# Performance work log

Hardware: AMD Instinct MI355X
Metric: run time of the kernel (lower is better)

## Reference

```python
import jax, jax.numpy as jnp
import numpy as np

B, C, H, W = 4, 64, 64, 64  # x shape; mask is (B,1,8H,8W)


def _conv(x, w, pad=0):
    return jax.lax.conv_general_dilated(
        x, w, (1, 1), [(pad, pad), (pad, pad)],
        dimension_numbers=('NCHW', 'OIHW', 'NCHW'))


def _inorm(x, eps=1e-5):  # InstanceNorm2d, affine=False, biased var (torch default)
    mu = x.mean(axis=(2, 3), keepdims=True)
    var = x.var(axis=(2, 3), keepdims=True)
    return (x - mu) * jax.lax.rsqrt(var + eps)


def _forward(x, mask, kconv_w1, kconv_w2, fs_w1, fs_w2, fs_b2, fs_fuse_w):
    b, c, h, w = x.shape
    n = h * w
    # MaxPool2d(8,8) then binarize
    m = jax.lax.reduce_window(mask, -jnp.inf, jax.lax.max,
                              (1, 1, 8, 8), (1, 1, 8, 8), 'VALID')
    m = (m > 0).astype(x.dtype)
    back = 1.0 - m
    # ResidualBlock K_conv (shared for K and Q paths in original code)
    y = jax.nn.relu(_inorm(_conv(x, kconv_w1, pad=1)))
    y = _inorm(_conv(y, kconv_w2, pad=1))
    kx = jax.nn.relu(y + x)
    # L2-normalized K/Q over channel dim
    K = (kx * back).reshape(b, c, n)
    K = K / (jnp.linalg.norm(K, axis=1, keepdims=True) + 1e-8)
    Q = (kx * m).reshape(b, c, n)
    Q = Q / (jnp.linalg.norm(Q, axis=1, keepdims=True) + 1e-8)
    V = (x * back).reshape(b, c, n)
    # cosine-similarity score map, temperature 20
    score = jnp.einsum('bcq,bck->bqk', Q, K) * 20.0  # (b, n_q, n_k)
    qm = m.reshape(b, 1, n)      # query mask (foreground)
    km = back.reshape(b, 1, n)   # key mask (background)
    NEG = -1000000.0
    validx = score + (1.0 - km) * NEG + (1.0 - qm.transpose(0, 2, 1)) * NEG
    att = jax.nn.softmax(validx, axis=-1) * (qm.transpose(0, 2, 1) * km)
    # att_fore[b,c,q] = sum_k V[b,c,k] * att[b,q,k]
    att_fore = jnp.einsum('bck,bqk->bcq', V, att).reshape(b, c, h, w)
    # Fusion_score
    feat1 = _conv(jnp.concatenate([x * m, att_fore * m], axis=1), fs_w1)
    s = jax.nn.sigmoid(_conv(feat1, fs_w2) + fs_b2[None, :, None, None])
    fused = _conv(jnp.concatenate([x * m, att_fore * m * (1.0 - s)], axis=1), fs_fuse_w)
    fs_out = fused * m + x * (1.0 - m)
    out = fs_out * m + x * (1.0 - m)
    # visualization attention mask
    visatt = att.sum(axis=1).reshape(b, 1, h, w)
    attmask = jnp.repeat(jnp.repeat(visatt, 8, axis=2), 8, axis=3)  # nearest upsample x8
    attmask = attmask / attmask.max()
    return out, attmask


def setup_inputs() -> dict:
    key = jax.random.key(0)
    ks = jax.random.split(key, 8)

    def wgt(k, shape, fan_in):
        return jax.random.normal(k, shape, jnp.float32) / np.sqrt(fan_in)

    x = jax.random.normal(ks[0], (B, C, H, W), jnp.float32)
    # sparse foreground mask so maxpool(8x8)>0 yields a mixed fg/bg mask
    mask = (jax.random.uniform(ks[1], (B, 1, H * 8, W * 8)) < 0.01).astype(jnp.float32)
    return dict(
        x=x, mask=mask,
        kconv_w1=wgt(ks[2], (C, C, 3, 3), C * 9),
        kconv_w2=wgt(ks[3], (C, C, 3, 3), C * 9),
        fs_w1=wgt(ks[4], (C, 2 * C, 1, 1), 2 * C),
        fs_w2=wgt(ks[5], (C, C, 1, 1), C),
        fs_b2=jnp.zeros((C,), jnp.float32),
        fs_fuse_w=wgt(ks[6], (C, 2 * C, 1, 1), 2 * C),
    )


def reference(x, mask, kconv_w1, kconv_w2, fs_w1, fs_w2, fs_b2, fs_fuse_w):
    return _forward(x, mask, kconv_w1, kconv_w2, fs_w1, fs_w2, fs_b2, fs_fuse_w)
```

## Files before the change

kernel.cpp:

```cpp
#include <hip/hip_runtime.h>
#include <hip/hip_bf16.h>

typedef __hip_bfloat16 bf16;
typedef __attribute__((ext_vector_type(8))) short short8;
typedef __attribute__((ext_vector_type(4))) float f32x4;
typedef __attribute__((ext_vector_type(16))) float f32x16;

#define BB 4
#define CC 64
#define NN 4096
#define MH 512
#define MW 512
#define LS 72
#define NPARTS 16
#define NDEN 32

#define WB_AFC  ((size_t)0)
#define WB_VIS  ((size_t)4259840)
#define WB_QIX  ((size_t)4325376)
#define WB_KIX  ((size_t)4390912)
#define WB_MFL  ((size_t)4456448)
#define WB_CNT  ((size_t)4472832)
#define WB_WT1  ((size_t)4476992)
#define WB_WT2  ((size_t)4550720)
#define WB_WFB  ((size_t)4624448)
#define WB_KC   ((size_t)5242880)
#define WB_XT   ((size_t)8388608)
#define WB_KXT  ((size_t)10485760)
#define WB_VC   ((size_t)12582912)
#define WB_QC   ((size_t)14680064)
#define WB_E    ((size_t)16777216)
#define EB_ELEM ((size_t)16777216)
#define WB_AFCP ((size_t)150994944)
#define WB_DENP ((size_t)218103808)
#define WB_VISP ((size_t)220200960)
#define WB_GST  ((size_t)220725248)

__device__ __forceinline__ float us2f(unsigned short u) { return __uint_as_float(((unsigned)u) << 16); }
__device__ __forceinline__ unsigned short f2bu(float f) {
  bf16 h = __float2bfloat16(f);
  return *(unsigned short*)&h;
}

__global__ __launch_bounds__(256) void k_pre(const float* __restrict__ x,
                                             const float* __restrict__ mask,
                                             const float* __restrict__ w1,
                                             const float* __restrict__ w2,
                                             const float* __restrict__ fw1,
                                             const float* __restrict__ fw2,
                                             const float* __restrict__ fwf,
                                             float* __restrict__ outp,
                                             unsigned short* __restrict__ xt,
                                             unsigned char* __restrict__ mfl,
                                             float* __restrict__ vis,
                                             unsigned int* __restrict__ vmaxb,
                                             unsigned short* __restrict__ wT1,
                                             unsigned short* __restrict__ wT2,
                                             unsigned short* __restrict__ wfb) {
  __shared__ float lx[64][65];
  int t = threadIdx.x;
  if (blockIdx.x < 256) {
    int b = blockIdx.x >> 6, p0 = (blockIdx.x & 63) * 64;
    const float* xb = x + (size_t)b * CC * NN + p0;
    float* ob = outp + (size_t)b * CC * NN + p0;
    for (int idx = t; idx < 4096; idx += 256) {
      int c = idx >> 6, j = idx & 63;
      float v = xb[c * NN + j];
      lx[j][c] = v;
      ob[c * NN + j] = v;
    }
    __syncthreads();
    unsigned short* xo = xt + ((size_t)b * NN + p0) * 64;
    for (int idx = t; idx < 2048; idx += 256) {
      int j = idx >> 5, c2 = (idx & 31) * 2;
      ushort2 w2v;
      w2v.x = f2bu(lx[j][c2]);
      w2v.y = f2bu(lx[j][c2 + 1]);
      *(ushort2*)&xo[j * 64 + c2] = w2v;
    }
  } else {
    int g = (blockIdx.x - 256) * 256 + t;
    int o = g >> 2, sub = g & 3;
    int b = o >> 12, p = o & 4095;
    int py = p >> 6, px = p & 63;
    const float* mb = mask + (size_t)b * MH * MW + (py * 8 + sub * 2) * MW + px * 8;
    float mx = 0.f;
    #pragma unroll
    for (int dy = 0; dy < 2; ++dy) {
      const float4* r4 = (const float4*)(mb + dy * MW);
      float4 a = r4[0], c = r4[1];
      mx = fmaxf(mx, fmaxf(fmaxf(a.x, a.y), fmaxf(a.z, a.w)));
      mx = fmaxf(mx, fmaxf(fmaxf(c.x, c.y), fmaxf(c.z, c.w)));
    }
    mx = fmaxf(mx, __shfl_xor(mx, 1));
    mx = fmaxf(mx, __shfl_xor(mx, 2));
    if (sub == 0) {
      mfl[o] = (mx > 0.f) ? 1 : 0;
      vis[o] = 0.f;
    }
    if (g == 0) vmaxb[0] = 0u;
    if (g < 36864) {
      int tap = g >> 12;
      int rem = g & 4095;
      int co = rem >> 6, ci = rem & 63;
      int src = (co * 64 + ci) * 9 + tap;
      wT1[g] = f2bu(w1[src]);
      wT2[g] = f2bu(w2[src]);
    } else if (g < 57344) {
      int j2 = g - 36864;
      if (j2 < 8192)       wfb[j2] = f2bu(fw1[j2]);
      else if (j2 < 12288) wfb[j2] = f2bu(fw2[j2 - 8192]);
      else                 wfb[j2] = f2bu(fwf[j2 - 12288]);
    }
  }
}

__global__ __launch_bounds__(256) void k_compact(const unsigned char* __restrict__ mfl,
                                                 int* __restrict__ qidx, int* __restrict__ kidx,
                                                 int* __restrict__ nq, int* __restrict__ nk) {
  int b = blockIdx.x;
  __shared__ unsigned char lm[4096];
  int t = threadIdx.x;
  *(uint4*)&lm[t * 16] = *(const uint4*)&mfl[b * NN + t * 16];
  __syncthreads();
  if (t >= 64) return;
  int lane = t;
  int qb = 0, kb = 0;
  #pragma unroll
  for (int it = 0; it < 64; ++it) {
    int p = it * 64 + lane;
    bool f = lm[p] != 0;
    unsigned long long bal = __ballot(f);
    int before = __popcll(bal & ((1ULL << lane) - 1ULL));
    if (f)  qidx[b * NN + qb + before] = p;
    if (!f) kidx[b * NN + kb + (lane - before)] = p;
    int cnt = __popcll(bal);
    qb += cnt; kb += 64 - cnt;
  }
  if (lane == 0) { nq[b] = qb; nk[b] = kb; }
}

template <bool NORM_IN>
__global__ __launch_bounds__(256) void k_convm(const unsigned short* __restrict__ src,
                                               const unsigned short* __restrict__ wT,
                                               const float* __restrict__ insum,
                                               const float* __restrict__ insq,
                                               unsigned short* __restrict__ dst,
                                               float* __restrict__ gsump,
                                               float* __restrict__ gsqp) {
  int b = blockIdx.y;
  int r = blockIdx.x;
  __shared__ unsigned short bx[198 * LS];
  __shared__ float nmean[64], ninv[64];
  int t = threadIdx.x;
  if (NORM_IN) {
    if (t < 64) {
      float s = 0.f, s2v = 0.f;
      #pragma unroll 8
      for (int r2 = 0; r2 < 64; ++r2) {
        s   += insum[((size_t)r2 * BB + b) * 64 + t];
        s2v += insq [((size_t)r2 * BB + b) * 64 + t];
      }
      float m = s * (1.f / NN);
      float v = fmaxf(s2v * (1.f / NN) - m * m, 0.f);
      nmean[t] = m; ninv[t] = rsqrtf(v + 1e-5f);
    }
    __syncthreads();
  }
  const unsigned short* sb = src + (size_t)b * NN * 64;
  for (int idx = t; idx < 198 * 8; idx += 256) {
    int row = idx >> 3, c8 = (idx & 7) * 8;
    int dy = row / 66;
    int cx = row - dy * 66 - 1;
    int rr = r + dy - 1;
    uint4 v = make_uint4(0u, 0u, 0u, 0u);
    if ((unsigned)rr < 64u && (unsigned)cx < 64u) {
      v = *(const uint4*)(sb + ((size_t)(rr * 64 + cx)) * 64 + c8);
      if (NORM_IN) {
        unsigned short* e = (unsigned short*)&v;
        #pragma unroll
        for (int j = 0; j < 8; ++j)
          e[j] = f2bu(fmaxf((us2f(e[j]) - nmean[c8 + j]) * ninv[c8 + j], 0.f));
      }
    }
    *(uint4*)&bx[row * LS + c8] = v;
  }
  __syncthreads();
  int lane = t & 63;
  int quad = lane >> 4, col = lane & 15;
  int qw = (t >> 6) * 16;
  f32x4 acc[4] = {{0.f,0.f,0.f,0.f},{0.f,0.f,0.f,0.f},{0.f,0.f,0.f,0.f},{0.f,0.f,0.f,0.f}};
  #pragma unroll
  for (int tap = 0; tap < 9; ++tap) {
    int dy = tap / 3, dx = tap - dy * 3 - 1;
    const unsigned short* wrow = wT + ((size_t)tap * 64 + qw + col) * 64;
    short8 a0 = *(const short8*)(wrow + quad * 8);
    short8 a1 = *(const short8*)(wrow + 32 + quad * 8);
    int rbase = dy * 66 + dx + 1;
    #pragma unroll
    for (int nt = 0; nt < 4; ++nt) {
      int row = rbase + nt * 16 + col;
      short8 b0 = *(const short8*)&bx[row * LS + quad * 8];
      short8 b1 = *(const short8*)&bx[row * LS + 32 + quad * 8];
      acc[nt] = __builtin_amdgcn_mfma_f32_16x16x32_bf16(a0, b0, acc[nt], 0, 0, 0);
      acc[nt] = __builtin_amdgcn_mfma_f32_16x16x32_bf16(a1, b1, acc[nt], 0, 0, 0);
    }
  }
  #pragma unroll
  for (int rr = 0; rr < 4; ++rr) {
    float s1 = acc[0][rr] + acc[1][rr] + acc[2][rr] + acc[3][rr];
    float s2 = acc[0][rr]*acc[0][rr] + acc[1][rr]*acc[1][rr]
             + acc[2][rr]*acc[2][rr] + acc[3][rr]*acc[3][rr];
    s1 += __shfl_xor(s1, 1); s2 += __shfl_xor(s2, 1);
    s1 += __shfl_xor(s1, 2); s2 += __shfl_xor(s2, 2);
    s1 += __shfl_xor(s1, 4); s2 += __shfl_xor(s2, 4);
    s1 += __shfl_xor(s1, 8); s2 += __shfl_xor(s2, 8);
    if (col == 0) {
      int co = qw + quad * 4 + rr;
      gsump[((size_t)r * BB + b) * 64 + co] = s1;
      gsqp [((size_t)r * BB + b) * 64 + co] = s2;
    }
  }
  __syncthreads();
  #pragma unroll
  for (int nt = 0; nt < 4; ++nt)
    #pragma unroll
    for (int rr = 0; rr < 4; ++rr)
      bx[(nt * 16 + col) * LS + qw + quad * 4 + rr] = f2bu(acc[nt][rr]);
  __syncthreads();
  unsigned short* db = dst + ((size_t)b * NN + r * 64) * 64;
  for (int idx = t; idx < 512; idx += 256) {
    int px = idx >> 3, c8 = (idx & 7) * 8;
    *(uint4*)(db + (size_t)px * 64 + c8) = *(const uint4*)&bx[px * LS + c8];
  }
}

__global__ __launch_bounds__(256) void k_knorm(unsigned short* __restrict__ kxt,
                                               const unsigned short* __restrict__ xt,
                                               const float* __restrict__ gsump,
                                               const float* __restrict__ gsqp) {
  int b = blockIdx.x >> 6;
  int p0 = (blockIdx.x & 63) * 64;
  __shared__ float m2[64], i2[64];
  int t = threadIdx.x;
  if (t < 64) {
    float s = 0.f, s2v = 0.f;
    #pragma unroll 8
    for (int r2 = 0; r2 < 64; ++r2) {
      s   += gsump[((size_t)r2 * BB + b) * 64 + t];
      s2v += gsqp [((size_t)r2 * BB + b) * 64 + t];
    }
    float m = s * (1.f / NN);
    float v = fmaxf(s2v * (1.f / NN) - m * m, 0.f);
    m2[t] = m; i2[t] = rsqrtf(v + 1e-5f);
  }
  __syncthreads();
  int px = t >> 2, c0 = (t & 3) * 16;
  size_t base = ((size_t)b * NN + p0 + px) * 64 + c0;
  unsigned short kv[16], xv[16];
  *(uint4*)&kv[0] = *(const uint4*)(kxt + base);
  *(uint4*)&kv[8] = *(const uint4*)(kxt + base + 8);
  *(uint4*)&xv[0] = *(const uint4*)(xt + base);
  *(uint4*)&xv[8] = *(const uint4*)(xt + base + 8);
  float v[16]; float ss = 0.f;
  #pragma unroll
  for (int j = 0; j < 16; ++j) {
    float f = fmaxf((us2f(kv[j]) - m2[c0 + j]) * i2[c0 + j] + us2f(xv[j]), 0.f);
    v[j] = f; ss += f * f;
  }
  ss += __shfl_xor(ss, 1);
  ss += __shfl_xor(ss, 2);
  float inv = 1.f / (sqrtf(ss) + 1e-8f);
  #pragma unroll
  for (int j = 0; j < 16; ++j) kv[j] = f2bu(v[j] * inv);
  *(uint4*)(kxt + base) = *(const uint4*)&kv[0];
  *(uint4*)(kxt + base + 8) = *(const uint4*)&kv[8];
}

__global__ __launch_bounds__(256) void k_gath(const unsigned short* __restrict__ khat,
                                              const unsigned short* __restrict__ xt,
                                              const int* __restrict__ qidx, const int* __restrict__ kidx,
                                              const int* __restrict__ nqv, const int* __restrict__ nkv,
                                              unsigned short* __restrict__ kc,
                                              unsigned short* __restrict__ vc,
                                              unsigned short* __restrict__ qc) {
  int b = blockIdx.y;
  int j0 = blockIdx.x * 64;
  int nqb = nqv[b], nkb = nkv[b];
  int NKP = (nkb + 63) & ~63, NQP = (nqb + 63) & ~63;
  bool dok = j0 < NKP, doq = j0 < NQP;
  if (!dok && !doq) return;
  __shared__ int li[128];
  int t = threadIdx.x;
  if (t < 64)       li[t]      = (j0 + t < nkb) ? kidx[b * NN + j0 + t] : -1;
  else if (t < 128) li[t - 64 + 64] = li[t - 64 + 64];
  if (t >= 64 && t < 128) li[t] = (j0 + (t - 64) < nqb) ? qidx[b * NN + j0 + (t - 64)] : -1;
  __syncthreads();
  const unsigned short* khb = khat + (size_t)b * NN * 64;
  const unsigned short* xtb = xt + (size_t)b * NN * 64;
  uint4 z = make_uint4(0u, 0u, 0u, 0u);
  for (int idx = t; idx < 512; idx += 256) {
    int row = idx >> 3, c8 = (idx & 7) * 8;
    size_t dsto = ((size_t)b * NN + j0 + row) * 64 + c8;
    if (dok) {
      int sk = li[row];
      *(uint4*)(kc + dsto) = (sk >= 0) ? *(const uint4*)(khb + (size_t)sk * 64 + c8) : z;
      *(uint4*)(vc + dsto) = (sk >= 0) ? *(const uint4*)(xtb + (size_t)sk * 64 + c8) : z;
    }
    if (doq) {
      int sq = li[64 + row];
      *(uint4*)(qc + dsto) = (sq >= 0) ? *(const uint4*)(khb + (size_t)sq * 64 + c8) : z;
    }
  }
}

__global__ __launch_bounds__(256) void k_att1(const unsigned short* __restrict__ kc,
                                              const unsigned short* __restrict__ vc,
                                              const unsigned short* __restrict__ qc,
                                              const int* __restrict__ nqv, const int* __restrict__ nkv,
                                              float* __restrict__ afc_part, float* __restrict__ den_part,
                                              unsigned short* __restrict__ eg) {
  int b = blockIdx.y;
  int nqb = nqv[b], nkb = nkv[b];
  int q0 = (blockIdx.x >> 4) * 64;
  int part = blockIdx.x & (NPARTS - 1);
  if (q0 >= nqb) return;
  int ntiles = (nkb + 63) >> 6;
  int nt_blk = (part < ntiles) ? ((ntiles - part + NPARTS - 1) >> 4) : 0;
  int NKP = (nkb + 63) & ~63;
  __shared__ unsigned short lk [64 * LS];
  __shared__ unsigned short lvT[64 * LS];
  __shared__ unsigned short le [64 * LS];
  int t = threadIdx.x;
  int wave = t >> 6, lane = t & 63;
  int l31 = lane & 31, lhi = lane >> 5;
  int qh = wave >> 1, kh = wave & 1;
  const unsigned short* kcb = kc + (size_t)b * NN * 64;
  const unsigned short* vcb = vc + (size_t)b * NN * 64;
  const unsigned short* qcb = qc + (size_t)b * NN * 64;
  unsigned short* egb = eg + (size_t)b * EB_ELEM;
  float* afcp = afc_part + (((size_t)part * BB + b) * NN) * 64;
  float* denp = den_part + (((size_t)(part * 2 + kh)) * BB + b) * NN;
  int qq_a = q0 + qh * 32 + l31;
  short8 aq[4];
  #pragma unroll
  for (int ks = 0; ks < 4; ++ks)
    aq[ks] = *(const short8*)(qcb + (size_t)qq_a * 64 + ks * 16 + lhi * 8);
  int klo = t >> 3, c8 = (t & 7) * 8, vcc = t & 7;
  uint4 g0, g1, g2, g3;
  auto issue_gather = [&](int it) {
    int j0 = (part + it * NPARTS) * 64;
    g0 = *(const uint4*)(kcb + (size_t)(j0 + klo) * 64 + c8);
    g1 = *(const uint4*)(kcb + (size_t)(j0 + klo + 32) * 64 + c8);
    g2 = *(const uint4*)(vcb + (size_t)(j0 + 2 * klo) * 64 + c8);
    g3 = *(const uint4*)(vcb + (size_t)(j0 + 2 * klo + 1) * 64 + c8);
  };
  if (nt_blk > 0) issue_gather(0);
  f32x16 pv, dsum;
  #pragma unroll
  for (int i = 0; i < 16; ++i) { pv[i] = 0.f; dsum[i] = 0.f; }
  for (int it = 0; it < nt_blk; ++it) {
    int j0 = (part + it * NPARTS) * 64;
    __syncthreads();
    *(uint4*)&lk[klo * LS + c8] = g0;
    *(uint4*)&lk[(klo + 32) * LS + c8] = g1;
    {
      const unsigned short* e0 = (const unsigned short*)&g2;
      const unsigned short* e1 = (const unsigned short*)&g3;
      int pbase = klo & 3, prun = klo >> 2;
      int pp = pbase + ((prun ^ vcc) << 2);
      #pragma unroll
      for (int jj = 0; jj < 8; ++jj) {
        unsigned int w2 = (unsigned)e0[jj] | ((unsigned)e1[jj] << 16);
        *(unsigned int*)&lvT[(c8 + jj) * LS + pp * 2] = w2;
      }
    }
    __syncthreads();
    if (it + 1 < nt_blk) issue_gather(it + 1);
    f32x16 s;
    #pragma unroll
    for (int i = 0; i < 16; ++i) s[i] = 0.f;
    #pragma unroll
    for (int ks = 0; ks < 4; ++ks) {
      short8 bk = *(const short8*)&lk[(kh * 32 + l31) * LS + ks * 16 + lhi * 8];
      s = __builtin_amdgcn_mfma_f32_32x32x16_bf16(aq[ks], bk, s, 0, 0, 0);
    }
    bool kval = (j0 + kh * 32 + l31) < nkb;
    #pragma unroll
    for (int reg = 0; reg < 16; ++reg) {
      float e = kval ? __expf(20.f * s[reg]) : 0.f;
      dsum[reg] += e;
      int row = (reg & 3) + 8 * (reg >> 2) + 4 * lhi;
      le[(qh * 32 + row) * LS + kh * 32 + l31] = f2bu(e);
    }
    __syncthreads();
    for (int idx = t; idx < 512; idx += 256) {
      int q = idx >> 3, cc8 = (idx & 7) * 8;
      if (q0 + q < nqb)
        *(uint4*)(egb + (size_t)(q0 + q) * NKP + j0 + cc8) = *(const uint4*)&le[q * LS + cc8];
    }
    int c = kh * 32 + l31;
    int c37 = (c >> 3) & 7;
    #pragma unroll
    for (int ks = 0; ks < 4; ++ks) {
      short8 a  = *(const short8*)&le[(qh * 32 + l31) * LS + ks * 16 + lhi * 8];
      int run = ks * 2 + lhi;
      short8 bv = *(const short8*)&lvT[c * LS + ((run ^ c37) << 3)];
      pv = __builtin_amdgcn_mfma_f32_32x32x16_bf16(a, bv, pv, 0, 0, 0);
    }
  }
  #pragma unroll
  for (int reg = 0; reg < 16; ++reg) {
    float v = dsum[reg];
    v += __shfl_xor(v, 1); v += __shfl_xor(v, 2); v += __shfl_xor(v, 4);
    v += __shfl_xor(v, 8); v += __shfl_xor(v, 16);
    int row = (reg & 3) + 8 * (reg >> 2) + 4 * lhi;
    int qq = q0 + qh * 32 + row;
    if (l31 == 0 && qq < nqb) denp[qq] = v;
  }
  #pragma unroll
  for (int reg = 0; reg < 16; ++reg) {
    int row = (reg & 3) + 8 * (reg >> 2) + 4 * lhi;
    int qq = q0 + qh * 32 + row;
    if (qq < nqb) afcp[(size_t)qq * 64 + kh * 32 + l31] = pv[reg];
  }
}

__global__ __launch_bounds__(256) void k_vis(const unsigned short* __restrict__ eg,
                                             const float* __restrict__ den_part,
                                             const int* __restrict__ nqv, const int* __restrict__ nkv,
                                             float* __restrict__ visp) {
  int b = blockIdx.z;
  int nqb = nqv[b], nkb = nkv[b];
  int k0 = blockIdx.x * 256;
  if (k0 >= nkb) return;
  int NKP = (nkb + 63) & ~63;
  int qpart = blockIdx.y;
  int qbeg = (qpart * nqb) >> 3;
  int qend = ((qpart + 1) * nqb) >> 3;
  __shared__ float wd[256];
  int t = threadIdx.x;
  int k = k0 + t;
  const unsigned short* eb = eg + (size_t)b * EB_ELEM;
  float acc = 0.f;
  for (int qc = qbeg; qc < qend; qc += 256) {
    __syncthreads();
    int qq = qc + t;
    float d = 0.f;
    if (qq < qend) {
      #pragma unroll
      for (int p2 = 0; p2 < NDEN; ++p2) d += den_part[((size_t)p2 * BB + b) * NN + qq];
    }
    wd[t] = (d > 0.f) ? 1.f / d : 0.f;
    __syncthreads();
    int lim = min(256, qend - qc);
    if (k < nkb) {
      const unsigned short* ep = eb + (size_t)qc * NKP + k;
      int j = 0;
      for (; j + 8 <= lim; j += 8) {
        #pragma unroll
        for (int u = 0; u < 8; ++u)
          acc += us2f(ep[(size_t)(j + u) * NKP]) * wd[j + u];
      }
      for (; j < lim; ++j)
        acc += us2f(ep[(size_t)j * NKP]) * wd[j];
    }
  }
  if (k < nkb) visp[((size_t)qpart * BB + b) * NN + k] = acc;
}

#define FS 136
__global__ __launch_bounds__(256) void k_fusionm(const unsigned short* __restrict__ xt,
                                                 const float* __restrict__ afc_part,
                                                 const float* __restrict__ den_part,
                                                 const int* __restrict__ qidx, const int* __restrict__ nqv,
                                                 const unsigned short* __restrict__ wall,
                                                 const float* __restrict__ b2,
                                                 float* __restrict__ outp) {
  int b = blockIdx.y;
  int nqb = nqv[b];
  int q0 = blockIdx.x * 64;
  if (q0 >= nqb) return;
  __shared__ unsigned short pxa[64 * FS];
  __shared__ unsigned short f1s[64 * LS];
  __shared__ int qpl[64];
  int t = threadIdx.x;
  int lane = t & 63;
  int quad = lane >> 4, col = lane & 15;
  int cb = (t >> 6) * 16;
  const int* qix = qidx + b * NN;
  const unsigned short* xtb = xt + (size_t)b * NN * 64;
  const unsigned short* w1b = wall;
  const unsigned short* w2b = wall + 8192;
  const unsigned short* wfb = wall + 12288;
  short8 a1[4], a2[2], af[4];
  #pragma unroll
  for (int kt = 0; kt < 4; ++kt) {
    a1[kt] = *(const short8*)&w1b[(cb + col) * 128 + kt * 32 + quad * 8];
    af[kt] = *(const short8*)&wfb[(cb + col) * 128 + kt * 32 + quad * 8];
  }
  #pragma unroll
  for (int kt = 0; kt < 2; ++kt)
    a2[kt] = *(const short8*)&w2b[(cb + col) * 64 + kt * 32 + quad * 8];
  float b2v[4];
  #pragma unroll
  for (int r = 0; r < 4; ++r) b2v[r] = b2[cb + quad * 4 + r];
  if (t < 64) qpl[t] = (q0 + t < nqb) ? qix[q0 + t] : -1;
  for (int idx = t; idx < 512; idx += 256) {
    int q = idx >> 3, c8 = (idx & 7) * 8;
    int qq = q0 + q;
    uint4 pv = make_uint4(0u, 0u, 0u, 0u);
    unsigned short pa8[8] = {0, 0, 0, 0, 0, 0, 0, 0};
    if (qq < nqb) {
      int qp = qix[qq];
      pv = *(const uint4*)(xtb + (size_t)qp * 64 + c8);
      float d = 0.f;
      #pragma unroll
      for (int p2 = 0; p2 < NDEN; ++p2)
        d += den_part[((size_t)p2 * BB + b) * NN + qq];
      float av[8];
      #pragma unroll
      for (int j = 0; j < 8; ++j) av[j] = 0.f;
      #pragma unroll
      for (int p2 = 0; p2 < NPARTS; ++p2) {
        const float4* ap4 = (const float4*)(afc_part + (((size_t)p2 * BB + b) * NN + qq) * 64 + c8);
        float4 u0 = ap4[0], u1 = ap4[1];
        av[0] += u0.x; av[1] += u0.y; av[2] += u0.z; av[3] += u0.w;
        av[4] += u1.x; av[5] += u1.y; av[6] += u1.z; av[7] += u1.w;
      }
      float invd = (d > 0.f) ? 1.f / d : 0.f;
      #pragma unroll
      for (int j = 0; j < 8; ++j) pa8[j] = f2bu(av[j] * invd);
    }
    *(uint4*)&pxa[q * FS + c8] = pv;
    *(uint4*)&pxa[q * FS + 64 + c8] = *(const uint4*)&pa8[0];
  }
  __syncthreads();
  #pragma unroll
  for (int qt = 0; qt < 4; ++qt) {
    f32x4 acc = {0.f, 0.f, 0.f, 0.f};
    #pragma unroll
    for (int kt = 0; kt < 4; ++kt) {
      short8 bfrag = *(const short8*)&pxa[(qt * 16 + col) * FS + kt * 32 + quad * 8];
      acc = __builtin_amdgcn_mfma_f32_16x16x32_bf16(a1[kt], bfrag, acc, 0, 0, 0);
    }
    #pragma unroll
    for (int r = 0; r < 4; ++r)
      f1s[(qt * 16 + col) * LS + cb + quad * 4 + r] = f2bu(acc[r]);
  }
  __syncthreads();
  #pragma unroll
  for (int qt = 0; qt < 4; ++qt) {
    f32x4 acc = {0.f, 0.f, 0.f, 0.f};
    #pragma unroll
    for (int kt = 0; kt < 2; ++kt) {
      short8 bfrag = *(const short8*)&f1s[(qt * 16 + col) * LS + kt * 32 + quad * 8];
      acc = __builtin_amdgcn_mfma_f32_16x16x32_bf16(a2[kt], bfrag, acc, 0, 0, 0);
    }
    #pragma unroll
    for (int r = 0; r < 4; ++r) {
      float sg = 1.f / (1.f + __expf(-(acc[r] + b2v[r])));
      int addr = (qt * 16 + col) * FS + 64 + cb + quad * 4 + r;
      pxa[addr] = f2bu(us2f(pxa[addr]) * (1.f - sg));
    }
  }
  __syncthreads();
  #pragma unroll
  for (int qt = 0; qt < 4; ++qt) {
    f32x4 acc = {0.f, 0.f, 0.f, 0.f};
    #pragma unroll
    for (int kt = 0; kt < 4; ++kt) {
      short8 bfrag = *(const short8*)&pxa[(qt * 16 + col) * FS + kt * 32 + quad * 8];
      acc = __builtin_amdgcn_mfma_f32_16x16x32_bf16(af[kt], bfrag, acc, 0, 0, 0);
    }
    int qp = qpl[qt * 16 + col];
    if (qp >= 0) {
      #pragma unroll
      for (int r = 0; r < 4; ++r)
        outp[((size_t)b * CC + cb + quad * 4 + r) * NN + qp] = acc[r];
    }
  }
}

__global__ __launch_bounds__(256) void k_vmax(const float* __restrict__ visp,
                                              const int* __restrict__ kidx,
                                              const int* __restrict__ nkv,
                                              float* __restrict__ vis,
                                              unsigned int* __restrict__ vmaxb) {
  int i = blockIdx.x * 256 + threadIdx.x;
  int b = i >> 12, k = i & 4095;
  float v = 0.f;
  if (k < nkv[b]) {
    #pragma unroll
    for (int p2 = 0; p2 < 8; ++p2) v += visp[((size_t)p2 * BB + b) * NN + k];
    vis[b * NN + kidx[b * NN + k]] = v;
  }
  #pragma unroll
  for (int off = 32; off > 0; off >>= 1) v = fmaxf(v, __shfl_down(v, off));
  if ((threadIdx.x & 63) == 0) atomicMax(vmaxb, __float_as_uint(v));
}

__global__ __launch_bounds__(256) void k_upsample(const float* __restrict__ vis,
                                                  const unsigned int* __restrict__ vmaxb,
                                                  float* __restrict__ out2) {
  int i4 = blockIdx.x * 256 + threadIdx.x;
  int b = i4 >> 16;
  int rem = i4 & 65535;
  int y = rem >> 7, x4 = (rem & 127) * 4;
  float vm = __uint_as_float(vmaxb[0]);
  if (!(vm > 0.f)) vm = 1.f;
  float v = vis[b * NN + (y >> 3) * 64 + (x4 >> 3)] / vm;
  ((float4*)out2)[i4] = make_float4(v, v, v, v);
}

extern "C" void kernel_launch(void* const* d_in, const int* in_sizes, int n_in,
                              void* d_out, int out_size, void* d_ws, size_t ws_size,
                              hipStream_t stream) {
  const float* x    = (const float*)d_in[0];
  const float* mask = (const float*)d_in[1];
  const float* w1   = (const float*)d_in[2];
  const float* w2c  = (const float*)d_in[3];
  const float* fsw1 = (const float*)d_in[4];
  const float* fsw2 = (const float*)d_in[5];
  const float* fsb2 = (const float*)d_in[6];
  const float* fswf = (const float*)d_in[7];
  float* out = (float*)d_out;
  char* wsb = (char*)d_ws;

  float* vis = (float*)(wsb + WB_VIS);
  int* qidx  = (int*)(wsb + WB_QIX);
  int* kidx  = (int*)(wsb + WB_KIX);
  unsigned char* mfl = (unsigned char*)(wsb + WB_MFL);
  int* nq = (int*)(wsb + WB_CNT);
  int* nk = nq + 4;
  unsigned int* vmaxb = (unsigned int*)(nq + 8);
  unsigned short* wT1 = (unsigned short*)(wsb + WB_WT1);
  unsigned short* wT2 = (unsigned short*)(wsb + WB_WT2);
  unsigned short* wall = (unsigned short*)(wsb + WB_WFB);
  unsigned short* y1t = (unsigned short*)(wsb + WB_AFC);
  unsigned short* xt  = (unsigned short*)(wsb + WB_XT);
  unsigned short* kxt = (unsigned short*)(wsb + WB_KXT);
  unsigned short* khat = kxt;
  unsigned short* kc  = (unsigned short*)(wsb + WB_KC);
  unsigned short* vc  = (unsigned short*)(wsb + WB_VC);
  unsigned short* qc  = (unsigned short*)(wsb + WB_QC);
  unsigned short* eg  = (unsigned short*)(wsb + WB_E);
  float* afc_part = (float*)(wsb + WB_AFCP);
  float* den_part = (float*)(wsb + WB_DENP);
  float* visp     = (float*)(wsb + WB_VISP);
  float* gsum1p = (float*)(wsb + WB_GST);
  float* gsq1p  = (float*)(wsb + WB_GST + 65536);
  float* gsum2p = (float*)(wsb + WB_GST + 131072);
  float* gsq2p  = (float*)(wsb + WB_GST + 196608);

  k_pre<<<512, 256, 0, stream>>>(x, mask, w1, w2c, fsw1, fsw2, fswf,
                                 out, xt, mfl, vis, vmaxb, wT1, wT2, wall);
  k_compact<<<4, 256, 0, stream>>>(mfl, qidx, kidx, nq, nk);
  k_convm<false><<<dim3(64, BB), 256, 0, stream>>>(xt, wT1, nullptr, nullptr, y1t, gsum1p, gsq1p);
  k_convm<true><<<dim3(64, BB), 256, 0, stream>>>(y1t, wT2, gsum1p, gsq1p, kxt, gsum2p, gsq2p);
  k_knorm<<<256, 256, 0, stream>>>(kxt, xt, gsum2p, gsq2p);
  k_gath<<<dim3(64, BB), 256, 0, stream>>>(khat, xt, qidx, kidx, nq, nk, kc, vc, qc);
  k_att1<<<dim3(64 * NPARTS, BB), 256, 0, stream>>>(kc, vc, qc, nq, nk, afc_part, den_part, eg);
  k_vis<<<dim3(16, 8, BB), 256, 0, stream>>>(eg, den_part, nq, nk, visp);
  k_fusionm<<<dim3(64, BB), 256, 0, stream>>>(xt, afc_part, den_part, qidx, nq, wall, fsb2, out);
  k_vmax<<<64, 256, 0, stream>>>(visp, kidx, nk, vis, vmaxb);
  k_upsample<<<1024, 256, 0, stream>>>(vis, vmaxb, out + 1048576);
}
```

Before: 175.8 us.

## Split attention kernel into single-wave 32-query blocks with bf16 partial outputs

The attention kernel moves from 4-wave blocks handling 64 queries to single-wave blocks handling 32 queries, each wave computing both key halves and both channel halves. This removes all __syncthreads barriers and raises the number of blocks. The partial attention-output buffer is stored as bf16 instead of fp32 to halve partial write and read traffic in the fusion kernel, and the denominator partial count drops from 32 to 16. In exchange, the register-prefetch gather pipelining is lost, K/V tiles are reloaded per 32-query block (twice the K/V traffic), and summing bf16 partials loses some precision.

```diff
diff --git a/kernel.cpp b/kernel.cpp
--- a/kernel.cpp
+++ b/kernel.cpp
@@ -13,7 +13,7 @@
 #define MW 512
 #define LS 72
 #define NPARTS 16
-#define NDEN 32
+#define NDEN 16
 
 #define WB_AFC  ((size_t)0)
 #define WB_VIS  ((size_t)4259840)
@@ -292,8 +292,7 @@
   if (!dok && !doq) return;
   __shared__ int li[128];
   int t = threadIdx.x;
-  if (t < 64)       li[t]      = (j0 + t < nkb) ? kidx[b * NN + j0 + t] : -1;
-  else if (t < 128) li[t - 64 + 64] = li[t - 64 + 64];
+  if (t < 64) li[t] = (j0 + t < nkb) ? kidx[b * NN + j0 + t] : -1;
   if (t >= 64 && t < 128) li[t] = (j0 + (t - 64) < nqb) ? qidx[b * NN + j0 + (t - 64)] : -1;
   __syncthreads();
   const unsigned short* khb = khat + (size_t)b * NN * 64;
@@ -314,15 +313,16 @@
   }
 }
 
-__global__ __launch_bounds__(256) void k_att1(const unsigned short* __restrict__ kc,
-                                              const unsigned short* __restrict__ vc,
-                                              const unsigned short* __restrict__ qc,
-                                              const int* __restrict__ nqv, const int* __restrict__ nkv,
-                                              float* __restrict__ afc_part, float* __restrict__ den_part,
-                                              unsigned short* __restrict__ eg) {
+__global__ __launch_bounds__(64) void k_att1(const unsigned short* __restrict__ kc,
+                                             const unsigned short* __restrict__ vc,
+                                             const unsigned short* __restrict__ qc,
+                                             const int* __restrict__ nqv, const int* __restrict__ nkv,
+                                             unsigned short* __restrict__ afc_part,
+                                             float* __restrict__ den_part,
+                                             unsigned short* __restrict__ eg) {
   int b = blockIdx.y;
   int nqb = nqv[b], nkb = nkv[b];
-  int q0 = (blockIdx.x >> 4) * 64;
+  int q0 = (blockIdx.x >> 4) * 32;
   int part = blockIdx.x & (NPARTS - 1);
   if (q0 >= nqb) return;
   int ntiles = (nkb + 63) >> 6;
@@ -330,83 +330,79 @@
   int NKP = (nkb + 63) & ~63;
   __shared__ unsigned short lk [64 * LS];
   __shared__ unsigned short lvT[64 * LS];
-  __shared__ unsigned short le [64 * LS];
-  int t = threadIdx.x;
-  int wave = t >> 6, lane = t & 63;
+  __shared__ unsigned short le [32 * LS];
+  int lane = threadIdx.x;
   int l31 = lane & 31, lhi = lane >> 5;
-  int qh = wave >> 1, kh = wave & 1;
   const unsigned short* kcb = kc + (size_t)b * NN * 64;
   const unsigned short* vcb = vc + (size_t)b * NN * 64;
   const unsigned short* qcb = qc + (size_t)b * NN * 64;
   unsigned short* egb = eg + (size_t)b * EB_ELEM;
-  float* afcp = afc_part + (((size_t)part * BB + b) * NN) * 64;
-  float* denp = den_part + (((size_t)(part * 2 + kh)) * BB + b) * NN;
-  int qq_a = q0 + qh * 32 + l31;
+  unsigned short* afcp = afc_part + (((size_t)part * BB + b) * NN) * 64;
+  float* denp = den_part + ((size_t)part * BB + b) * NN;
   short8 aq[4];
   #pragma unroll
   for (int ks = 0; ks < 4; ++ks)
-    aq[ks] = *(const short8*)(qcb + (size_t)qq_a * 64 + ks * 16 + lhi * 8);
-  int klo = t >> 3, c8 = (t & 7) * 8, vcc = t & 7;
-  uint4 g0, g1, g2, g3;
-  auto issue_gather = [&](int it) {
-    int j0 = (part + it * NPARTS) * 64;
-    g0 = *(const uint4*)(kcb + (size_t)(j0 + klo) * 64 + c8);
-    g1 = *(const uint4*)(kcb + (size_t)(j0 + klo + 32) * 64 + c8);
-    g2 = *(const uint4*)(vcb + (size_t)(j0 + 2 * klo) * 64 + c8);
-    g3 = *(const uint4*)(vcb + (size_t)(j0 + 2 * klo + 1) * 64 + c8);
-  };
-  if (nt_blk > 0) issue_gather(0);
-  f32x16 pv, dsum;
-  #pragma unroll
-  for (int i = 0; i < 16; ++i) { pv[i] = 0.f; dsum[i] = 0.f; }
+    aq[ks] = *(const short8*)(qcb + (size_t)(q0 + l31) * 64 + ks * 16 + lhi * 8);
+  f32x16 pv0, pv1, dsum;
+  #pragma unroll
+  for (int i = 0; i < 16; ++i) { pv0[i] = 0.f; pv1[i] = 0.f; dsum[i] = 0.f; }
   for (int it = 0; it < nt_blk; ++it) {
     int j0 = (part + it * NPARTS) * 64;
-    __syncthreads();
-    *(uint4*)&lk[klo * LS + c8] = g0;
-    *(uint4*)&lk[(klo + 32) * LS + c8] = g1;
-    {
-      const unsigned short* e0 = (const unsigned short*)&g2;
-      const unsigned short* e1 = (const unsigned short*)&g3;
-      int pbase = klo & 3, prun = klo >> 2;
-      int pp = pbase + ((prun ^ vcc) << 2);
+    #pragma unroll
+    for (int sub = 0; sub < 4; ++sub) {
+      int tt = sub * 64 + lane;
+      int klo = tt >> 3, c8 = (tt & 7) * 8, vcc = tt & 7;
+      *(uint4*)&lk[klo * LS + c8] = *(const uint4*)(kcb + (size_t)(j0 + klo) * 64 + c8);
+      *(uint4*)&lk[(klo + 32) * LS + c8] = *(const uint4*)(kcb + (size_t)(j0 + klo + 32) * 64 + c8);
+      uint4 v0 = *(const uint4*)(vcb + (size_t)(j0 + 2 * klo) * 64 + c8);
+      uint4 v1 = *(const uint4*)(vcb + (size_t)(j0 + 2 * klo + 1) * 64 + c8);
+      const unsigned short* e0 = (const unsigned short*)&v0;
+      const unsigned short* e1 = (const unsigned short*)&v1;
+      int pp = (klo & 3) + (((klo >> 2) ^ vcc) << 2);
       #pragma unroll
       for (int jj = 0; jj < 8; ++jj) {
         unsigned int w2 = (unsigned)e0[jj] | ((unsigned)e1[jj] << 16);
         *(unsigned int*)&lvT[(c8 + jj) * LS + pp * 2] = w2;
       }
     }
-    __syncthreads();
-    if (it + 1 < nt_blk) issue_gather(it + 1);
-    f32x16 s;
-    #pragma unroll
-    for (int i = 0; i < 16; ++i) s[i] = 0.f;
-    #pragma unroll
-    for (int ks = 0; ks < 4; ++ks) {
-      short8 bk = *(const short8*)&lk[(kh * 32 + l31) * LS + ks * 16 + lhi * 8];
-      s = __builtin_amdgcn_mfma_f32_32x32x16_bf16(aq[ks], bk, s, 0, 0, 0);
-    }
-    bool kval = (j0 + kh * 32 + l31) < nkb;
-    #pragma unroll
-    for (int reg = 0; reg < 16; ++reg) {
-      float e = kval ? __expf(20.f * s[reg]) : 0.f;
-      dsum[reg] += e;
-      int row = (reg & 3) + 8 * (reg >> 2) + 4 * lhi;
-      le[(qh * 32 + row) * LS + kh * 32 + l31] = f2bu(e);
-    }
-    __syncthreads();
-    for (int idx = t; idx < 512; idx += 256) {
+    #pragma unroll
+    for (int kh = 0; kh < 2; ++kh) {
+      f32x16 s;
+      #pragma unroll
+      for (int i = 0; i < 16; ++i) s[i] = 0.f;
+      #pragma unroll
+      for (int ks = 0; ks < 4; ++ks) {
+        short8 bk = *(const short8*)&lk[(kh * 32 + l31) * LS + ks * 16 + lhi * 8];
+        s = __builtin_amdgcn_mfma_f32_32x32x16_bf16(aq[ks], bk, s, 0, 0, 0);
+      }
+      bool kval = (j0 + kh * 32 + l31) < nkb;
+      #pragma unroll
+      for (int reg = 0; reg < 16; ++reg) {
+        float e = kval ? __expf(20.f * s[reg]) : 0.f;
+        dsum[reg] += e;
+        int row = (reg & 3) + 8 * (reg >> 2) + 4 * lhi;
+        le[row * LS + kh * 32 + l31] = f2bu(e);
+      }
+    }
+    #pragma unroll
+    for (int sub = 0; sub < 4; ++sub) {
+      int idx = sub * 64 + lane;
       int q = idx >> 3, cc8 = (idx & 7) * 8;
       if (q0 + q < nqb)
         *(uint4*)(egb + (size_t)(q0 + q) * NKP + j0 + cc8) = *(const uint4*)&le[q * LS + cc8];
     }
-    int c = kh * 32 + l31;
-    int c37 = (c >> 3) & 7;
-    #pragma unroll
-    for (int ks = 0; ks < 4; ++ks) {
-      short8 a  = *(const short8*)&le[(qh * 32 + l31) * LS + ks * 16 + lhi * 8];
-      int run = ks * 2 + lhi;
-      short8 bv = *(const short8*)&lvT[c * LS + ((run ^ c37) << 3)];
-      pv = __builtin_amdgcn_mfma_f32_32x32x16_bf16(a, bv, pv, 0, 0, 0);
+    #pragma unroll
+    for (int ch = 0; ch < 2; ++ch) {
+      int c = ch * 32 + l31;
+      int c37 = (c >> 3) & 7;
+      #pragma unroll
+      for (int ks = 0; ks < 4; ++ks) {
+        short8 a  = *(const short8*)&le[l31 * LS + ks * 16 + lhi * 8];
+        int run = ks * 2 + lhi;
+        short8 bv = *(const short8*)&lvT[c * LS + ((run ^ c37) << 3)];
+        if (ch == 0) pv0 = __builtin_amdgcn_mfma_f32_32x32x16_bf16(a, bv, pv0, 0, 0, 0);
+        else         pv1 = __builtin_amdgcn_mfma_f32_32x32x16_bf16(a, bv, pv1, 0, 0, 0);
+      }
     }
   }
   #pragma unroll
@@ -415,14 +411,17 @@
     v += __shfl_xor(v, 1); v += __shfl_xor(v, 2); v += __shfl_xor(v, 4);
     v += __shfl_xor(v, 8); v += __shfl_xor(v, 16);
     int row = (reg & 3) + 8 * (reg >> 2) + 4 * lhi;
-    int qq = q0 + qh * 32 + row;
+    int qq = q0 + row;
     if (l31 == 0 && qq < nqb) denp[qq] = v;
   }
   #pragma unroll
   for (int reg = 0; reg < 16; ++reg) {
     int row = (reg & 3) + 8 * (reg >> 2) + 4 * lhi;
-    int qq = q0 + qh * 32 + row;
-    if (qq < nqb) afcp[(size_t)qq * 64 + kh * 32 + l31] = pv[reg];
+    int qq = q0 + row;
+    if (qq < nqb) {
+      afcp[(size_t)qq * 64 + l31]      = f2bu(pv0[reg]);
+      afcp[(size_t)qq * 64 + 32 + l31] = f2bu(pv1[reg]);
+    }
   }
 }
 
@@ -471,7 +470,7 @@
 
 #define FS 136
 __global__ __launch_bounds__(256) void k_fusionm(const unsigned short* __restrict__ xt,
-                                                 const float* __restrict__ afc_part,
+                                                 const unsigned short* __restrict__ afc_part,
                                                  const float* __restrict__ den_part,
                                                  const int* __restrict__ qidx, const int* __restrict__ nqv,
                                                  const unsigned short* __restrict__ wall,
@@ -523,10 +522,10 @@
       for (int j = 0; j < 8; ++j) av[j] = 0.f;
       #pragma unroll
       for (int p2 = 0; p2 < NPARTS; ++p2) {
-        const float4* ap4 = (const float4*)(afc_part + (((size_t)p2 * BB + b) * NN + qq) * 64 + c8);
-        float4 u0 = ap4[0], u1 = ap4[1];
-        av[0] += u0.x; av[1] += u0.y; av[2] += u0.z; av[3] += u0.w;
-        av[4] += u1.x; av[5] += u1.y; av[6] += u1.z; av[7] += u1.w;
+        const uint4 u = *(const uint4*)(afc_part + (((size_t)p2 * BB + b) * NN + qq) * 64 + c8);
+        const unsigned short* e8 = (const unsigned short*)&u;
+        #pragma unroll
+        for (int j = 0; j < 8; ++j) av[j] += us2f(e8[j]);
       }
       float invd = (d > 0.f) ? 1.f / d : 0.f;
       #pragma unroll
@@ -645,7 +644,7 @@
   unsigned short* vc  = (unsigned short*)(wsb + WB_VC);
   unsigned short* qc  = (unsigned short*)(wsb + WB_QC);
   unsigned short* eg  = (unsigned short*)(wsb + WB_E);
-  float* afc_part = (float*)(wsb + WB_AFCP);
+  unsigned short* afc_part = (unsigned short*)(wsb + WB_AFCP);
   float* den_part = (float*)(wsb + WB_DENP);
   float* visp     = (float*)(wsb + WB_VISP);
   float* gsum1p = (float*)(wsb + WB_GST);
@@ -660,7 +659,7 @@
   k_convm<true><<<dim3(64, BB), 256, 0, stream>>>(y1t, wT2, gsum1p, gsq1p, kxt, gsum2p, gsq2p);
   k_knorm<<<256, 256, 0, stream>>>(kxt, xt, gsum2p, gsq2p);
   k_gath<<<dim3(64, BB), 256, 0, stream>>>(khat, xt, qidx, kidx, nq, nk, kc, vc, qc);
-  k_att1<<<dim3(64 * NPARTS, BB), 256, 0, stream>>>(kc, vc, qc, nq, nk, afc_part, den_part, eg);
+  k_att1<<<dim3(128 * NPARTS, BB), 64, 0, stream>>>(kc, vc, qc, nq, nk, afc_part, den_part, eg);
   k_vis<<<dim3(16, 8, BB), 256, 0, stream>>>(eg, den_part, nq, nk, visp);
   k_fusionm<<<dim3(64, BB), 256, 0, stream>>>(xt, afc_part, den_part, qidx, nq, wall, fsb2, out);
   k_vmax<<<64, 256, 0, stream>>>(visp, kidx, nk, vis, vmaxb);
```

Result: no change. 172.6 us (-1.9%).
